# Performance work log

Measured on AMD Instinct MI355X. Metric: run time of the kernel, lower is better.

The kernel has to match this reference:

```python
import jax, jax.numpy as jnp
import numpy as np

DIM = 1024
N_HEADS = 16
HEAD_DIM = DIM // N_HEADS
B, T = 4, 2048


def setup_inputs() -> dict:
    key = jax.random.key(0)
    k_x, k_cos, k_sin, k_wqkv, k_wout = jax.random.split(key, 5)
    x = jax.random.normal(k_x, (B, T, DIM), dtype=jnp.float32)
    # rotary tables indexed by position, half the head dim
    pos = jnp.arange(T, dtype=jnp.float32)[:, None]
    inv_freq = 1.0 / (10000.0 ** (jnp.arange(0, HEAD_DIM, 2, dtype=jnp.float32) / HEAD_DIM))
    ang = pos * inv_freq[None, :]  # [T, HEAD_DIM//2]
    cos = jnp.cos(ang)
    sin = jnp.sin(ang)
    mask = jnp.zeros((T, T), dtype=jnp.float32)
    Wqkv = jax.random.normal(k_wqkv, (3 * DIM, DIM), dtype=jnp.float32) * 0.02
    Wout = jax.random.normal(k_wout, (DIM, DIM), dtype=jnp.float32) * 0.02
    return {"x": x, "cos": cos, "sin": sin, "mask": mask, "Wqkv": Wqkv, "Wout": Wout}


def _apply_rope(t, cos, sin):
    # t: [B, T, H, D]; cos/sin: [T, D//2]
    d = t.shape[-1]
    t1, t2 = t[..., : d // 2], t[..., d // 2 :]
    c = cos[: t.shape[1]][None, :, None, :]
    s = sin[: t.shape[1]][None, :, None, :]
    return jnp.concatenate([t1 * c - t2 * s, t1 * s + t2 * c], axis=-1)


def reference(x, cos, sin, mask, Wqkv, Wout):
    Bx, Tx, C = x.shape
    scale = HEAD_DIM ** -0.5
    qkv = (x @ Wqkv.T).reshape(Bx, Tx, 3, N_HEADS, HEAD_DIM)
    q, k, v = qkv[:, :, 0], qkv[:, :, 1], qkv[:, :, 2]
    q = _apply_rope(q, cos, sin)
    k = _apply_rope(k, cos, sin)
    attn = jnp.einsum("bthd,bshd->bhts", q, k) * scale  # [B, H, T, T]
    attn = attn + mask[None, None, :, :]
    p = jax.nn.softmax(attn, axis=-1)
    out = jnp.einsum("bhts,bshd->bthd", p, v).reshape(Bx, Tx, C)
    return out @ Wout.T
```

## Files before the change

### kernel.cpp

```cpp
#include <hip/hip_runtime.h>
#include <math.h>

#define DIMC   1024
#define NHEADS 16
#define HD     64
#define BATCH  4
#define SEQ    2048
#define MROWS  (BATCH * SEQ)
#define QKVC   (3 * DIMC)
#define QSCALE 0.1803368801111204f

typedef __bf16 bf16x8 __attribute__((ext_vector_type(8)));
typedef float  f32x4  __attribute__((ext_vector_type(4)));
typedef short  s16x4  __attribute__((ext_vector_type(4)));
typedef unsigned short us;

#define MFMA16(a, b, c) __builtin_amdgcn_mfma_f32_16x16x32_bf16(a, b, c, 0, 0, 0)

__device__ __forceinline__ f32x4 mfma16x16x16(s16x4 a, s16x4 b, f32x4 c) {
#if __has_builtin(__builtin_amdgcn_mfma_f32_16x16x16bf16_1k)
    return __builtin_amdgcn_mfma_f32_16x16x16bf16_1k(a, b, c, 0, 0, 0);
#else
    asm volatile("v_mfma_f32_16x16x16_bf16 %0, %1, %2, %0"
                 : "+v"(c) : "v"(a), "v"(b));
    return c;
#endif
}

__device__ __forceinline__ void async16(const void* g, void* l) {
    __builtin_amdgcn_global_load_lds(
        (const __attribute__((address_space(1))) void*)g,
        (__attribute__((address_space(3))) void*)l, 16, 0, 0);
}

__device__ __forceinline__ bf16x8 ldsfrag(const us* p) {
    union { int4 q; bf16x8 v; } u;
    u.q = *(const int4*)p;
    return u.v;
}

__device__ __forceinline__ s16x4 ldsfrag64(const us* p) {
    union { uint2 q; s16x4 v; } u;
    u.q = *(const uint2*)p;
    return u.v;
}

__device__ __forceinline__ bf16x8 gfrag(const us* __restrict__ p) {
    union { int4 q; bf16x8 v; } u;
    u.q = *(const int4*)p;
    return u.v;
}

__device__ __forceinline__ us bf16_rn(float f) {
    unsigned int u = __builtin_bit_cast(unsigned int, f);
    u += 0x7fffu + ((u >> 16) & 1u);
    return (us)(u >> 16);
}

__device__ __forceinline__ float fast_exp2(float x) {
#if __has_builtin(__builtin_amdgcn_exp2f)
    return __builtin_amdgcn_exp2f(x);
#else
    return __expf(x * 0.6931471805599453f);
#endif
}

__device__ __forceinline__ s16x4 pack4t(float a, float b, float c, float d) {
    union { unsigned u[2]; s16x4 v; } z;
    z.u[0] = __builtin_amdgcn_perm(__builtin_bit_cast(unsigned, b),
                                   __builtin_bit_cast(unsigned, a), 0x07060302);
    z.u[1] = __builtin_amdgcn_perm(__builtin_bit_cast(unsigned, d),
                                   __builtin_bit_cast(unsigned, c), 0x07060302);
    return z.v;
}

#define NX (MROWS * DIMC)
#define NW (QKVC * DIMC)
#define NO (DIMC * DIMC)
#define NC (SEQ * 32)
__global__ __launch_bounds__(256) void cast3_bf16(const float* __restrict__ x,
                                                  const float* __restrict__ wq,
                                                  const float* __restrict__ wo,
                                                  const float* __restrict__ cosb,
                                                  const float* __restrict__ sinb,
                                                  us* __restrict__ xb,
                                                  us* __restrict__ wqb,
                                                  us* __restrict__ wob,
                                                  float* __restrict__ cs2) {
    int i = (blockIdx.x * 256 + threadIdx.x) * 4;
    const float* src;
    us* dst;
    if (i < NX)                { src = x  + i;             dst = xb  + i; }
    else if (i < NX + NW)      { src = wq + (i - NX);      dst = wqb + (i - NX); }
    else if (i < NX + NW + NO) { src = wo + (i - NX - NW); dst = wob + (i - NX - NW); }
    else {
        int p0 = i - (NX + NW + NO);
        if (p0 >= NC) return;
        float4 c4 = *(const float4*)(cosb + p0);
        float4 s4 = *(const float4*)(sinb + p0);
        float4 o0 = {c4.x, s4.x, c4.y, s4.y};
        float4 o1 = {c4.z, s4.z, c4.w, s4.w};
        *(float4*)(cs2 + 2 * p0)     = o0;
        *(float4*)(cs2 + 2 * p0 + 4) = o1;
        return;
    }
    float4 v = *(const float4*)src;
    ushort4 o = {bf16_rn(v.x), bf16_rn(v.y), bf16_rn(v.z), bf16_rn(v.w)};
    *(ushort4*)dst = o;
}

template <int MODE>
__global__ __launch_bounds__(256) void gemm_bt(const us* __restrict__ A,
                                               const us* __restrict__ B,
                                               void* __restrict__ Cv,
                                               const float* __restrict__ cs2,
                                               int M, int N, int K) {
    __shared__ __align__(16) us As[128 * 32];
    __shared__ __align__(16) us Bs[128 * 32];

    const int tid  = threadIdx.x;
    const int lane = tid & 63, w = tid >> 6;
    const int col  = lane & 15, quad = lane >> 4;
    const int m0   = blockIdx.y * 128, n0 = blockIdx.x * 128;
    const int wm   = (w >> 1) * 64,   wn = (w & 1) * 64;

    const int srow = w * 32 + (lane >> 2);
    const int scol = (lane & 3) * 8;
    const us* Ag = A + (size_t)(m0 + srow) * K + scol;
    const us* Bg = B + (size_t)(n0 + srow) * K + scol;
    us* Asl = As + w * 1024 + lane * 8;
    us* Bsl = Bs + w * 1024 + lane * 8;

    f32x4 acc[4][4] = {};

    for (int k0 = 0; k0 < K; k0 += 32) {
        __syncthreads();
        async16(Ag + k0, Asl);
        async16(Ag + (size_t)16 * K + k0, Asl + 512);
        async16(Bg + k0, Bsl);
        async16(Bg + (size_t)16 * K + k0, Bsl + 512);
        __syncthreads();

        bf16x8 af[4], bfr[4];
#pragma unroll
        for (int mt = 0; mt < 4; ++mt)
            af[mt] = ldsfrag(As + (wm + mt * 16 + col) * 32 + quad * 8);
#pragma unroll
        for (int nt = 0; nt < 4; ++nt)
            bfr[nt] = ldsfrag(Bs + (wn + nt * 16 + col) * 32 + quad * 8);
#pragma unroll
        for (int mt = 0; mt < 4; ++mt)
#pragma unroll
            for (int nt = 0; nt < 4; ++nt)
                acc[mt][nt] = MFMA16(af[mt], bfr[nt], acc[mt][nt]);
    }

    if constexpr (MODE == 1) {
        us* C = (us*)Cv;
        const int gcol0 = n0 + wn;
        const bool is_v = (gcol0 >= 2 * DIMC);
        const float f = (gcol0 < DIMC) ? QSCALE : 1.0f;
#pragma unroll
        for (int mt = 0; mt < 4; ++mt) {
#pragma unroll
            for (int r = 0; r < 4; ++r) {
                const int grow = m0 + wm + mt * 16 + quad * 4 + r;
                if (is_v) {
#pragma unroll
                    for (int nt = 0; nt < 4; ++nt)
                        C[(size_t)grow * N + gcol0 + nt * 16 + col] =
                            bf16_rn(acc[mt][nt][r]);
                } else {
                    const int t = grow & (SEQ - 1);
#pragma unroll
                    for (int nt = 0; nt < 2; ++nt) {
                        const int d1 = nt * 16 + col;
                        const float2 cs = ((const float2*)cs2)[t * 32 + d1];
                        const float v1 = acc[mt][nt][r];
                        const float v2 = acc[mt][nt + 2][r];
                        C[(size_t)grow * N + gcol0 + d1]      = bf16_rn((v1 * cs.x - v2 * cs.y) * f);
                        C[(size_t)grow * N + gcol0 + d1 + 32] = bf16_rn((v1 * cs.y + v2 * cs.x) * f);
                    }
                }
            }
        }
    } else {
        float* C = (float*)Cv;
#pragma unroll
        for (int mt = 0; mt < 4; ++mt)
#pragma unroll
            for (int nt = 0; nt < 4; ++nt)
#pragma unroll
                for (int r = 0; r < 4; ++r)
                    C[(size_t)(m0 + wm + mt * 16 + quad * 4 + r) * N +
                      n0 + wn + nt * 16 + col] = acc[mt][nt][r];
    }
}

__global__ __launch_bounds__(256) void transpose_v(const us* __restrict__ qkv,
                                                   us* __restrict__ vt) {
    __shared__ us L[64][66];
    const int tid = threadIdx.x;
    const int bh = blockIdx.y, b = bh >> 4, h = bh & 15;
    const int t0 = blockIdx.x * 64;

    {
        const int tr = tid >> 2, dc = (tid & 3) * 16;
        const us* src = qkv + (size_t)(b * SEQ + t0 + tr) * QKVC + 2 * DIMC + h * HD + dc;
        *(int4*)&L[tr][dc]     = *(const int4*)src;
        *(int4*)&L[tr][dc + 8] = *(const int4*)(src + 8);
    }
    __syncthreads();
    {
        const int d = tid >> 2, tc = (tid & 3) * 16;
        unsigned int wb[8];
#pragma unroll
        for (int i = 0; i < 8; ++i)
            wb[i] = (unsigned int)L[tc + 2 * i][d] |
                    ((unsigned int)L[tc + 2 * i + 1][d] << 16);
        us* dst = vt + ((size_t)bh * HD + d) * SEQ + t0 + tc;
        *(int4*)dst       = make_int4(wb[0], wb[1], wb[2], wb[3]);
        *(int4*)(dst + 8) = make_int4(wb[4], wb[5], wb[6], wb[7]);
    }
}

__global__ __launch_bounds__(256, 2) void attn_mfma(const us* __restrict__ qkv,
                                                    const us* __restrict__ vt,
                                                    us* __restrict__ outb) {
    __shared__ __align__(16) us Ks[2 * 64 * 64];
    __shared__ __align__(16) us Vs[2 * 64 * 64];

    const int tid  = threadIdx.x;
    const int lane = tid & 63, w = tid >> 6;
    const int col  = lane & 15, quad = lane >> 4;

    const int f  = blockIdx.y * gridDim.x + blockIdx.x;
    const int c  = (f & 7) * 64 + (f >> 3);
    const int bh = c >> 3, b = bh >> 4, h = bh & 15;
    const int t0 = (c & 7) * 256;

    const int r8 = lane >> 3;
    const int cs = ((lane & 7) ^ r8) * 8;

    const int sw0 = ((quad ^ (col & 7)) << 3);
    const int sw4 = sw0 ^ 32;
    const int e2 = quad >> 1, o4 = (quad & 1) * 4, cm = col & 7;

    const us* qb = qkv + (size_t)b * SEQ * QKVC + h * HD;

    bf16x8 aq[4][2];
#pragma unroll
    for (int s = 0; s < 4; ++s)
#pragma unroll
        for (int hf = 0; hf < 2; ++hf)
            aq[s][hf] = gfrag(qb + (size_t)(t0 + s * 64 + w * 16 + col) * QKVC +
                              hf * 32 + quad * 8);

    const us* kg0 = qkv + (size_t)(b * SEQ + w * 16 + r8) * QKVC + DIMC + h * HD + cs;
    const us* vg0 = vt + ((size_t)bh * HD + w * 16 + r8) * SEQ + cs;
    us* kl = Ks + w * 1024 + lane * 8;
    us* vl = Vs + w * 1024 + lane * 8;

    union { us u[4]; s16x4 v; } ones4;
#pragma unroll
    for (int i = 0; i < 4; ++i) ones4.u[i] = 0x3F80;

    f32x4 o_acc[4][4] = {};
    f32x4 lacc[4] = {};

    async16(kg0, kl);
    async16(kg0 + (size_t)8 * QKVC, kl + 512);
    async16(vg0, vl);
    async16(vg0 + (size_t)8 * SEQ, vl + 512);
    asm volatile("s_waitcnt vmcnt(0)" ::: "memory");
    __builtin_amdgcn_s_barrier();
    __builtin_amdgcn_sched_barrier(0);

    int cur = 0;
    for (int s0 = 0; s0 < SEQ; s0 += 64) {
        if (s0 + 64 < SEQ) {
            const int nb = (cur ^ 1) << 12;
            async16(kg0 + (size_t)(s0 + 64) * QKVC, kl + nb);
            async16(kg0 + (size_t)(s0 + 72) * QKVC, kl + nb + 512);
            async16(vg0 + (s0 + 64), vl + nb);
            async16(vg0 + (s0 + 64) + (size_t)8 * SEQ, vl + nb + 512);
        }

        const us* Kb = Ks + (cur << 12);
        const us* Vb = Vs + (cur << 12);

        bf16x8 bk[4][2];
        s16x4  bv[4][4];
#pragma unroll
        for (int nt = 0; nt < 4; ++nt) {
            bk[nt][0] = ldsfrag(Kb + (nt * 16 + col) * 64 + sw0);
            bk[nt][1] = ldsfrag(Kb + (nt * 16 + col) * 64 + sw4);
#pragma unroll
            for (int dt = 0; dt < 4; ++dt)
                bv[nt][dt] = ldsfrag64(Vb + (dt * 16 + col) * 64 +
                                       (((nt * 2 + e2) ^ cm) << 3) + o4);
        }

        f32x4 st[4] = {};
#pragma unroll
        for (int nt = 0; nt < 4; ++nt) {
            st[nt] = MFMA16(bk[nt][0], aq[0][0], st[nt]);
            st[nt] = MFMA16(bk[nt][1], aq[0][1], st[nt]);
        }
#pragma unroll
        for (int s = 0; s < 4; ++s) {
            f32x4 stn[4] = {};
            if (s < 3) {
#pragma unroll
                for (int nt = 0; nt < 4; ++nt) {
                    stn[nt] = MFMA16(bk[nt][0], aq[s + 1][0], stn[nt]);
                    stn[nt] = MFMA16(bk[nt][1], aq[s + 1][1], stn[nt]);
                }
            }
            s16x4 ap[4];
#pragma unroll
            for (int nt = 0; nt < 4; ++nt)
                ap[nt] = pack4t(fast_exp2(st[nt][0]), fast_exp2(st[nt][1]),
                                fast_exp2(st[nt][2]), fast_exp2(st[nt][3]));
#pragma unroll
            for (int nt = 0; nt < 4; ++nt)
                lacc[s] = mfma16x16x16(ap[nt], ones4.v, lacc[s]);
#pragma unroll
            for (int dt = 0; dt < 4; ++dt)
#pragma unroll
                for (int nt = 0; nt < 4; ++nt)
                    o_acc[s][dt] = mfma16x16x16(ap[nt], bv[nt][dt], o_acc[s][dt]);
#pragma unroll
            for (int nt = 0; nt < 4; ++nt) st[nt] = stn[nt];
        }

        asm volatile("s_waitcnt vmcnt(0)" ::: "memory");
        __builtin_amdgcn_s_barrier();
        __builtin_amdgcn_sched_barrier(0);
        cur ^= 1;
    }

#pragma unroll
    for (int s = 0; s < 4; ++s) {
        float linv[4];
#pragma unroll
        for (int r = 0; r < 4; ++r) linv[r] = __builtin_amdgcn_rcpf(lacc[s][r]);
#pragma unroll
        for (int dt = 0; dt < 4; ++dt)
#pragma unroll
            for (int r = 0; r < 4; ++r) {
                const int t = t0 + s * 64 + w * 16 + quad * 4 + r;
                const int d = h * HD + dt * 16 + col;
                outb[(size_t)(b * SEQ + t) * DIMC + d] = bf16_rn(o_acc[s][dt][r] * linv[r]);
            }
    }
}

extern "C" void kernel_launch(void* const* d_in, const int* in_sizes, int n_in,
                              void* d_out, int out_size, void* d_ws, size_t ws_size,
                              hipStream_t stream) {
    const float* x    = (const float*)d_in[0];
    const float* cosb = (const float*)d_in[1];
    const float* sinb = (const float*)d_in[2];
    const float* Wqkv = (const float*)d_in[4];
    const float* Wout = (const float*)d_in[5];
    float* out = (float*)d_out;

    us* xb    = (us*)d_ws;
    us* wqkb  = xb + (size_t)MROWS * DIMC;
    us* woutb = wqkb + (size_t)QKVC * DIMC;
    us* qkvb  = woutb + (size_t)DIMC * DIMC;
    us* vtb   = qkvb + (size_t)MROWS * QKVC;
    us* aob   = vtb + (size_t)BATCH * NHEADS * HD * SEQ;
    float* cs2 = (float*)(aob + (size_t)MROWS * DIMC);

    cast3_bf16<<<(NX + NW + NO + NC) / 1024, 256, 0, stream>>>(
        x, Wqkv, Wout, cosb, sinb, xb, wqkb, woutb, cs2);

    gemm_bt<1><<<dim3(QKVC / 128, MROWS / 128), 256, 0, stream>>>(
        xb, wqkb, qkvb, cs2, MROWS, QKVC, DIMC);

    transpose_v<<<dim3(SEQ / 64, BATCH * NHEADS), 256, 0, stream>>>(qkvb, vtb);

    attn_mfma<<<dim3(SEQ / 256, BATCH * NHEADS), 256, 0, stream>>>(qkvb, vtb, aob);

    gemm_bt<0><<<dim3(DIMC / 128, MROWS / 128), 256, 0, stream>>>(
        aob, woutb, out, nullptr, MROWS, DIMC, DIMC);
}
```

Before: 311.3 us.

## Rewrite projection GEMMs with 256x128 tiles, double-buffered LDS, swizzle and XCD mapping

Both projection GEMMs move to a new 512-thread kernel with 256x128 output tiles and a K-step of 64. Next-tile loads are double-buffered so async global-to-LDS copies overlap the MFMA work, and an XOR swizzle on LDS columns is meant to cut bank conflicts. Blocks are remapped so each XCD gets a contiguous group of M rows, improving L2 reuse, and MFMA sections run at raised wave priority. K is hardcoded to 1024 and the LDS footprint grows to 96KB per block, which limits occupancy.

```diff
diff --git a/kernel.cpp b/kernel.cpp
--- a/kernel.cpp
+++ b/kernel.cpp
@@ -109,57 +109,84 @@
     *(ushort4*)dst = o;
 }
 
-template <int MODE>
-__global__ __launch_bounds__(256) void gemm_bt(const us* __restrict__ A,
-                                               const us* __restrict__ B,
-                                               void* __restrict__ Cv,
-                                               const float* __restrict__ cs2,
-                                               int M, int N, int K) {
-    __shared__ __align__(16) us As[128 * 32];
-    __shared__ __align__(16) us Bs[128 * 32];
+template <int MODE, int NCOLS, int NBLK>
+__global__ __launch_bounds__(512, 2) void gemm256(const us* __restrict__ A,
+                                                  const us* __restrict__ B,
+                                                  void* __restrict__ Cv,
+                                                  const float* __restrict__ cs2) {
+    __shared__ __align__(16) us As[2][256 * 64];
+    __shared__ __align__(16) us Bs[2][128 * 64];
 
     const int tid  = threadIdx.x;
     const int lane = tid & 63, w = tid >> 6;
     const int col  = lane & 15, quad = lane >> 4;
-    const int m0   = blockIdx.y * 128, n0 = blockIdx.x * 128;
-    const int wm   = (w >> 1) * 64,   wn = (w & 1) * 64;
-
-    const int srow = w * 32 + (lane >> 2);
-    const int scol = (lane & 3) * 8;
-    const us* Ag = A + (size_t)(m0 + srow) * K + scol;
-    const us* Bg = B + (size_t)(n0 + srow) * K + scol;
-    us* Asl = As + w * 1024 + lane * 8;
-    us* Bsl = Bs + w * 1024 + lane * 8;
+    const int r8   = lane >> 3, c8 = lane & 7;
+    const int wm   = (w >> 1) * 64, wn = (w & 1) * 64;
+
+    const int f    = blockIdx.y * gridDim.x + blockIdx.x;
+    const int xcd  = f & 7, idx = f >> 3;
+    const int m0   = (xcd * 4 + idx / NBLK) * 256;
+    const int n0   = (idx % NBLK) * 128;
+
+    const us* Ag = A + (size_t)(m0 + w * 8 + r8) * 1024 + (c8 ^ r8) * 8;
+    const us* Bg = B + (size_t)(n0 + w * 8 + r8) * 1024 + (c8 ^ r8) * 8;
+    us* Ad = &As[0][0] + w * 512 + lane * 8;
+    us* Bd = &Bs[0][0] + w * 512 + lane * 8;
+
+    auto stage = [&](int kt, int bb) __attribute__((always_inline)) {
+        const us* ag = Ag + kt * 64;
+        us* ad = Ad + bb * (256 * 64);
+#pragma unroll
+        for (int i = 0; i < 4; ++i)
+            async16(ag + (size_t)i * 64 * 1024, ad + i * 4096);
+        const us* bg = Bg + kt * 64;
+        us* bd = Bd + bb * (128 * 64);
+#pragma unroll
+        for (int i = 0; i < 2; ++i)
+            async16(bg + (size_t)i * 64 * 1024, bd + i * 4096);
+    };
 
     f32x4 acc[4][4] = {};
 
-    for (int k0 = 0; k0 < K; k0 += 32) {
-        __syncthreads();
-        async16(Ag + k0, Asl);
-        async16(Ag + (size_t)16 * K + k0, Asl + 512);
-        async16(Bg + k0, Bsl);
-        async16(Bg + (size_t)16 * K + k0, Bsl + 512);
-        __syncthreads();
-
-        bf16x8 af[4], bfr[4];
-#pragma unroll
-        for (int mt = 0; mt < 4; ++mt)
-            af[mt] = ldsfrag(As + (wm + mt * 16 + col) * 32 + quad * 8);
-#pragma unroll
-        for (int nt = 0; nt < 4; ++nt)
-            bfr[nt] = ldsfrag(Bs + (wn + nt * 16 + col) * 32 + quad * 8);
-#pragma unroll
-        for (int mt = 0; mt < 4; ++mt)
+    stage(0, 0);
+    asm volatile("s_waitcnt vmcnt(0)" ::: "memory");
+    __builtin_amdgcn_s_barrier();
+    __builtin_amdgcn_sched_barrier(0);
+
+    const int swz = col & 7;
+    for (int kt = 0; kt < 16; ++kt) {
+        if (kt + 1 < 16) stage(kt + 1, (kt + 1) & 1);
+        const us* Ab = &As[kt & 1][0];
+        const us* Bb = &Bs[kt & 1][0];
+#pragma unroll
+        for (int kk = 0; kk < 2; ++kk) {
+            bf16x8 af[4], bf[4];
+#pragma unroll
+            for (int mt = 0; mt < 4; ++mt)
+                af[mt] = ldsfrag(Ab + (wm + mt * 16 + col) * 64 +
+                                 (((kk * 4 + quad) ^ swz) * 8));
 #pragma unroll
             for (int nt = 0; nt < 4; ++nt)
-                acc[mt][nt] = MFMA16(af[mt], bfr[nt], acc[mt][nt]);
+                bf[nt] = ldsfrag(Bb + (wn + nt * 16 + col) * 64 +
+                                 (((kk * 4 + quad) ^ swz) * 8));
+            __builtin_amdgcn_s_setprio(1);
+#pragma unroll
+            for (int mt = 0; mt < 4; ++mt)
+#pragma unroll
+                for (int nt = 0; nt < 4; ++nt)
+                    acc[mt][nt] = MFMA16(af[mt], bf[nt], acc[mt][nt]);
+            __builtin_amdgcn_s_setprio(0);
+        }
+        asm volatile("s_waitcnt vmcnt(0)" ::: "memory");
+        __builtin_amdgcn_s_barrier();
+        __builtin_amdgcn_sched_barrier(0);
     }
 
     if constexpr (MODE == 1) {
         us* C = (us*)Cv;
         const int gcol0 = n0 + wn;
         const bool is_v = (gcol0 >= 2 * DIMC);
-        const float f = (gcol0 < DIMC) ? QSCALE : 1.0f;
+        const float fq = (gcol0 < DIMC) ? QSCALE : 1.0f;
 #pragma unroll
         for (int mt = 0; mt < 4; ++mt) {
 #pragma unroll
@@ -168,7 +195,7 @@
                 if (is_v) {
 #pragma unroll
                     for (int nt = 0; nt < 4; ++nt)
-                        C[(size_t)grow * N + gcol0 + nt * 16 + col] =
+                        C[(size_t)grow * NCOLS + gcol0 + nt * 16 + col] =
                             bf16_rn(acc[mt][nt][r]);
                 } else {
                     const int t = grow & (SEQ - 1);
@@ -178,8 +205,8 @@
                         const float2 cs = ((const float2*)cs2)[t * 32 + d1];
                         const float v1 = acc[mt][nt][r];
                         const float v2 = acc[mt][nt + 2][r];
-                        C[(size_t)grow * N + gcol0 + d1]      = bf16_rn((v1 * cs.x - v2 * cs.y) * f);
-                        C[(size_t)grow * N + gcol0 + d1 + 32] = bf16_rn((v1 * cs.y + v2 * cs.x) * f);
+                        C[(size_t)grow * NCOLS + gcol0 + d1]      = bf16_rn((v1 * cs.x - v2 * cs.y) * fq);
+                        C[(size_t)grow * NCOLS + gcol0 + d1 + 32] = bf16_rn((v1 * cs.y + v2 * cs.x) * fq);
                     }
                 }
             }
@@ -192,7 +219,7 @@
             for (int nt = 0; nt < 4; ++nt)
 #pragma unroll
                 for (int r = 0; r < 4; ++r)
-                    C[(size_t)(m0 + wm + mt * 16 + quad * 4 + r) * N +
+                    C[(size_t)(m0 + wm + mt * 16 + quad * 4 + r) * NCOLS +
                       n0 + wn + nt * 16 + col] = acc[mt][nt][r];
     }
 }
@@ -377,13 +404,13 @@
     cast3_bf16<<<(NX + NW + NO + NC) / 1024, 256, 0, stream>>>(
         x, Wqkv, Wout, cosb, sinb, xb, wqkb, woutb, cs2);
 
-    gemm_bt<1><<<dim3(QKVC / 128, MROWS / 128), 256, 0, stream>>>(
-        xb, wqkb, qkvb, cs2, MROWS, QKVC, DIMC);
+    gemm256<1, QKVC, QKVC / 128><<<dim3(QKVC / 128, MROWS / 256), 512, 0, stream>>>(
+        xb, wqkb, qkvb, cs2);
 
     transpose_v<<<dim3(SEQ / 64, BATCH * NHEADS), 256, 0, stream>>>(qkvb, vtb);
 
     attn_mfma<<<dim3(SEQ / 256, BATCH * NHEADS), 256, 0, stream>>>(qkvb, vtb, aob);
 
-    gemm_bt<0><<<dim3(DIMC / 128, MROWS / 128), 256, 0, stream>>>(
-        aob, woutb, out, nullptr, MROWS, DIMC, DIMC);
-}
+    gemm256<0, DIMC, DIMC / 128><<<dim3(DIMC / 128, MROWS / 256), 512, 0, stream>>>(
+        aob, woutb, out, nullptr);
+}
```

Result: faster. 304.8 us (-2.1%).
